# Kernel tuning notes

Measured on AMD Instinct MI355X. Metric: run time of the kernel, lower is better.

## Reference

```python
import jax, jax.numpy as jnp
import numpy as np

EPS = 1e-5  # matches module default eps


def setup_inputs() -> dict:
    key = jax.random.key(0)
    n, F = 4096, 256
    k1, k2, k3, k4, k5 = jax.random.split(key, 5)
    # Orthonormal eigenbasis (eigh of a symmetric Laplacian yields orthogonal V)
    V = jnp.linalg.qr(jax.random.normal(k1, (n, n), dtype=jnp.float32))[0]
    # Nonnegative Laplacian spectrum with lam[0] = 0 (module asserts sqrtlam[0] ~ 0)
    lam = jnp.sort(jax.random.uniform(k2, (n,), dtype=jnp.float32) * 4.0)
    lam = lam.at[0].set(0.0)
    x = jax.random.normal(k3, (n, F, 1), dtype=jnp.float32)
    y = jax.random.normal(k4, (n, F, 1), dtype=jnp.float32)
    t = jnp.float32(0.7)
    return {"x": x, "y": y, "t": t, "lam": lam, "V": V}


def reference(x, y, t, lam, V):
    # safe_sqrt: clamp tiny negatives (|lam|<eps) to zero before sqrt
    sqrtlam = jnp.sqrt(jnp.maximum(lam, 0.0))
    # P1 spectrum: cos(t * sqrt(lam))
    c = jnp.cos(t * sqrtlam)
    # P2 spectrum: sin(t*s)/s with limit t as s->0 (safe_P2_eigh)
    small = jnp.abs(sqrtlam) < EPS
    safe_s = jnp.where(small, 1.0, sqrtlam)
    p2 = jnp.where(small, t, jnp.sin(t * safe_s) / safe_s)

    def apply_spectral(d, sig):
        # (V diag(d) V^T) @ sig, contracted over node axis; sig: [n, F, C]
        vt_sig = jnp.einsum('ji,jfc->ifc', V, sig)          # V^T @ sig
        return jnp.einsum('ij,jfc->ifc', V, d[:, None, None] * vt_sig)

    # res1 + res2: P1 @ x + P2 @ y (the scatter-add message passing with all
    # nonzeros of the dense P matrices is exactly this dense mat-vec)
    return apply_spectral(c, x) + apply_spectral(p2, y)
```

## Files before the change

### kernel.cpp

```cpp
#include <hip/hip_runtime.h>

typedef __attribute__((ext_vector_type(8))) short short8;
typedef __attribute__((ext_vector_type(8))) unsigned short ushort8v;
typedef __attribute__((ext_vector_type(4))) float f32x4;

#define N_NODES 4096
#define N_FEAT  256

__device__ __forceinline__ unsigned short f2bf(float f) {
  union { float f; unsigned u; } a; a.f = f;
  unsigned r = a.u + 0x7FFFu + ((a.u >> 16) & 1u);
  return (unsigned short)(r >> 16);
}

__device__ __forceinline__ float bf2f(unsigned short u) {
  union { unsigned u; float f; } a; a.u = ((unsigned)u) << 16;
  return a.f;
}

__device__ __forceinline__ void gload_lds16(const void* g, void* l) {
  __builtin_amdgcn_global_load_lds(
      (const __attribute__((address_space(1))) void*)g,
      (__attribute__((address_space(3))) void*)l, 16, 0, 0);
}

__global__ __launch_bounds__(256) void prep_v_k(const float* __restrict__ V,
                                                unsigned short* __restrict__ Vbf,
                                                unsigned short* __restrict__ Vt) {
  __shared__ unsigned short tile[64][72];
  const int t = threadIdx.x;
  const int r = t >> 2, q = t & 3;
  const int gr = blockIdx.y * 64 + r;
  const int gc0 = blockIdx.x * 64;
#pragma unroll
  for (int i = 0; i < 4; ++i) {
    int c = q * 4 + i * 16;
    float4 v = *(const float4*)&V[(size_t)gr * N_NODES + gc0 + c];
    ushort4 u; u.x = f2bf(v.x); u.y = f2bf(v.y); u.z = f2bf(v.z); u.w = f2bf(v.w);
    *(ushort4*)&Vbf[(size_t)gr * N_NODES + gc0 + c] = u;
    tile[c + 0][r] = u.x; tile[c + 1][r] = u.y; tile[c + 2][r] = u.z; tile[c + 3][r] = u.w;
  }
  __syncthreads();
  const int r2 = t >> 2;
#pragma unroll
  for (int j = 0; j < 2; ++j) {
    int ms = q * 8 + j * 32;
    ushort8v u = *(const ushort8v*)&tile[r2][ms];
    *(ushort8v*)&Vt[(size_t)(gc0 + r2) * N_NODES + blockIdx.y * 64 + ms] = u;
  }
}

__global__ __launch_bounds__(256) void prep_xy_k(const float* __restrict__ x,
                                                 const float* __restrict__ y,
                                                 unsigned short* __restrict__ S2T) {
  __shared__ unsigned short tx[64][72];
  __shared__ unsigned short ty[64][72];
  const int t = threadIdx.x;
  const int r = t >> 2, q = t & 3;
  const int gj = blockIdx.y * 64 + r;
  const int gf0 = blockIdx.x * 64;
#pragma unroll
  for (int i = 0; i < 4; ++i) {
    int c = q * 4 + i * 16;
    float4 vx = *(const float4*)&x[(size_t)gj * N_FEAT + gf0 + c];
    float4 vy = *(const float4*)&y[(size_t)gj * N_FEAT + gf0 + c];
    tx[c + 0][r] = f2bf(vx.x); tx[c + 1][r] = f2bf(vx.y);
    tx[c + 2][r] = f2bf(vx.z); tx[c + 3][r] = f2bf(vx.w);
    ty[c + 0][r] = f2bf(vy.x); ty[c + 1][r] = f2bf(vy.y);
    ty[c + 2][r] = f2bf(vy.z); ty[c + 3][r] = f2bf(vy.w);
  }
  __syncthreads();
  const int f2 = t >> 2;
#pragma unroll
  for (int j = 0; j < 2; ++j) {
    int js = q * 8 + j * 32;
    ushort8v ux = *(const ushort8v*)&tx[f2][js];
    ushort8v uy = *(const ushort8v*)&ty[f2][js];
    *(ushort8v*)&S2T[(size_t)(2 * (gf0 + f2) + 0) * N_NODES + blockIdx.y * 64 + js] = ux;
    *(ushort8v*)&S2T[(size_t)(2 * (gf0 + f2) + 1) * N_NODES + blockIdx.y * 64 + js] = uy;
  }
}

template <int NTB>
__global__ __launch_bounds__(256, 3) void gemm_swz(const unsigned short* __restrict__ A,
                                                   const unsigned short* __restrict__ B,
                                                   unsigned short* __restrict__ part,
                                                   int K, int Kc, int Nn, size_t MN) {
  __shared__ unsigned short As[2][128 * 64];
  __shared__ unsigned short Bs[2][64 * 64];
  const int t = threadIdx.x;
  const int lane = t & 63, w = t >> 6;

  const unsigned L = blockIdx.x;
  const unsigned cx = L & 7u, j = L >> 3;
  const unsigned ntile = j & ((1u << NTB) - 1u);
  const unsigned group = cx * (128u >> NTB) + (j >> NTB);
  const unsigned mtile = group & 31u;
  const unsigned zz = group >> 5u;

  const int wr = (w >> 1) * 64;
  const int wc = (w & 1) * 32;
  const int l15 = lane & 15;
  const int lhi = lane >> 4;

  const size_t kbase = (size_t)zz * Kc;
  const size_t srcoff = (size_t)(lane >> 3) * K * 2 + (size_t)(((lane & 7) ^ (lane >> 3)) << 4);

  const char* Ag = (const char*)(A + (size_t)mtile * 128 * K + kbase);
  const char* Bg = (const char*)(B + (size_t)ntile * 64 * K + kbase);

  f32x4 acc[4][2];
#pragma unroll
  for (int mi = 0; mi < 4; ++mi)
#pragma unroll
    for (int ni = 0; ni < 2; ++ni) acc[mi][ni] = (f32x4){0.f, 0.f, 0.f, 0.f};

  auto STAGE = [&](int kt, int cur) {
    const size_t ko = (size_t)kt * 128;
#pragma unroll
    for (int q = 0; q < 4; ++q)
      gload_lds16(Ag + (size_t)(w * 4 + q) * 8 * K * 2 + srcoff + ko,
                  &As[cur][(w * 4 + q) * 512]);
#pragma unroll
    for (int q = 0; q < 2; ++q)
      gload_lds16(Bg + (size_t)(w * 2 + q) * 8 * K * 2 + srcoff + ko,
                  &Bs[cur][(w * 2 + q) * 512]);
  };

  auto COMPUTE = [&](int cur) {
    short8 a[4][2], b[2][2];
#pragma unroll
    for (int mi = 0; mi < 4; ++mi) {
      const int ar = wr + mi * 16 + l15;
#pragma unroll
      for (int ks = 0; ks < 2; ++ks)
        a[mi][ks] = *(const short8*)((const char*)&As[cur][0] + (size_t)ar * 128 +
                                     ((((ks << 2) | lhi) ^ (ar & 7)) << 4));
    }
#pragma unroll
    for (int ni = 0; ni < 2; ++ni) {
      const int br = wc + ni * 16 + l15;
#pragma unroll
      for (int ks = 0; ks < 2; ++ks)
        b[ni][ks] = *(const short8*)((const char*)&Bs[cur][0] + (size_t)br * 128 +
                                     ((((ks << 2) | lhi) ^ (br & 7)) << 4));
    }
#pragma unroll
    for (int ks = 0; ks < 2; ++ks)
#pragma unroll
      for (int mi = 0; mi < 4; ++mi)
#pragma unroll
        for (int ni = 0; ni < 2; ++ni)
          acc[mi][ni] = __builtin_amdgcn_mfma_f32_16x16x32_bf16(a[mi][ks], b[ni][ks],
                                                                acc[mi][ni], 0, 0, 0);
  };

  const int nkt = Kc >> 6;
  STAGE(0, 0);
  __syncthreads();
  int cur = 0;
  for (int kt = 0; kt < nkt - 1; ++kt) {
    STAGE(kt + 1, cur ^ 1);
    COMPUTE(cur);
    __syncthreads();
    cur ^= 1;
  }
  COMPUTE(cur);

  unsigned short* po = part + (size_t)zz * MN;
  const int m0 = mtile * 128 + wr + lhi * 4;
  const int n0 = ntile * 64 + wc + l15;
#pragma unroll
  for (int mi = 0; mi < 4; ++mi)
#pragma unroll
    for (int ni = 0; ni < 2; ++ni)
#pragma unroll
      for (int r = 0; r < 4; ++r)
        po[(size_t)(m0 + mi * 16 + r) * Nn + n0 + ni * 16] = f2bf(acc[mi][ni][r]);
}

__global__ __launch_bounds__(256) void reduce1_k(const unsigned short* __restrict__ part,
                                                 const float* __restrict__ lam,
                                                 const float* __restrict__ tp,
                                                 unsigned short* __restrict__ Zt) {
  __shared__ unsigned short zt[64][72];
  const int t = threadIdx.x;
  const int r = t >> 2, q = t & 3;
  const int m = blockIdx.y * 64 + r;
  const int n0 = blockIdx.x * 128;
  const float tv = tp[0];
  const float s = sqrtf(fmaxf(lam[m], 0.f));
  const float cv = cosf(tv * s);
  const float pv = (s < 1e-5f) ? tv : (sinf(tv * s) / s);
  float acc[16];
#pragma unroll
  for (int i = 0; i < 16; ++i) acc[i] = 0.f;
  for (int ks = 0; ks < 4; ++ks) {
    const unsigned short* p = part + ((size_t)ks * N_NODES + m) * 512 + n0;
#pragma unroll
    for (int i = 0; i < 8; ++i) {
      ushort4 u = *(const ushort4*)&p[q * 4 + i * 16];
      acc[2 * i + 0] += cv * bf2f(u.x) + pv * bf2f(u.y);
      acc[2 * i + 1] += cv * bf2f(u.z) + pv * bf2f(u.w);
    }
  }
#pragma unroll
  for (int i = 0; i < 8; ++i) {
    int f = q * 2 + i * 8;
    zt[f + 0][r] = f2bf(acc[2 * i + 0]);
    zt[f + 1][r] = f2bf(acc[2 * i + 1]);
  }
  __syncthreads();
  const int f2 = t >> 2;
  const int gf = blockIdx.x * 64 + f2;
#pragma unroll
  for (int w = 0; w < 2; ++w) {
    int js = q * 8 + w * 32;
    ushort8v u = *(const ushort8v*)&zt[f2][js];
    *(ushort8v*)&Zt[(size_t)gf * N_NODES + blockIdx.y * 64 + js] = u;
  }
}

__global__ __launch_bounds__(256) void reduce2_k(const unsigned short* __restrict__ part,
                                                 float* __restrict__ out) {
  const size_t e = ((size_t)blockIdx.x * 256 + threadIdx.x) * 4;
  float4 s = {0.f, 0.f, 0.f, 0.f};
#pragma unroll
  for (int ks = 0; ks < 8; ++ks) {
    ushort4 u = *(const ushort4*)&part[(size_t)ks * N_NODES * N_FEAT + e];
    s.x += bf2f(u.x); s.y += bf2f(u.y); s.z += bf2f(u.z); s.w += bf2f(u.w);
  }
  *(float4*)&out[e] = s;
}

extern "C" void kernel_launch(void* const* d_in, const int* in_sizes, int n_in,
                              void* d_out, int out_size, void* d_ws, size_t ws_size,
                              hipStream_t stream) {
  const float* x   = (const float*)d_in[0];
  const float* y   = (const float*)d_in[1];
  const float* tp  = (const float*)d_in[2];
  const float* lam = (const float*)d_in[3];
  const float* V   = (const float*)d_in[4];

  char* w = (char*)d_ws;
  unsigned short* Vbf  = (unsigned short*)w; w += (size_t)N_NODES * N_NODES * 2;
  unsigned short* Vtbf = (unsigned short*)w; w += (size_t)N_NODES * N_NODES * 2;
  unsigned short* S2T  = (unsigned short*)w; w += (size_t)512 * N_NODES * 2;
  unsigned short* Zt   = (unsigned short*)w; w += (size_t)N_FEAT * N_NODES * 2;
  unsigned short* partb = (unsigned short*)w; w += (size_t)4 * N_NODES * 512 * 2;

  prep_v_k<<<dim3(N_NODES / 64, N_NODES / 64), 256, 0, stream>>>(V, Vbf, Vtbf);
  prep_xy_k<<<dim3(N_FEAT / 64, N_NODES / 64), 256, 0, stream>>>(x, y, S2T);
  gemm_swz<3><<<1024, 256, 0, stream>>>(Vtbf, S2T, partb, N_NODES, 1024, 512,
                                        (size_t)N_NODES * 512);
  reduce1_k<<<dim3(512 / 128, N_NODES / 64), 256, 0, stream>>>(partb, lam, tp, Zt);
  gemm_swz<2><<<1024, 256, 0, stream>>>(Vbf, Zt, partb, N_NODES, 512, N_FEAT,
                                        (size_t)N_NODES * N_FEAT);
  reduce2_k<<<(N_NODES * N_FEAT) / 1024, 256, 0, stream>>>(partb, (float*)d_out);
}
```

Before: 192.6 us.

## Enlarge GEMM tiles to 128x128, drop double buffering, double split-K factor

The GEMM block tile grows from 128x64 to 128x128, so each wave now computes a 64x64 output with 16 accumulators and gets more reuse from each LDS load. The LDS double buffer is replaced by a single buffer with load, sync, compute, sync per k-step, which removes overlap between the global-to-LDS copy and the MFMA work. To keep 1024 blocks, the K split doubles (8 and 16 partials), so both reduce kernels read twice as many bf16 partial buffers and the partial workspace doubles.

```diff
diff --git a/kernel.cpp b/kernel.cpp
--- a/kernel.cpp
+++ b/kernel.cpp
@@ -86,20 +86,21 @@
                                                    const unsigned short* __restrict__ B,
                                                    unsigned short* __restrict__ part,
                                                    int K, int Kc, int Nn, size_t MN) {
-  __shared__ unsigned short As[2][128 * 64];
-  __shared__ unsigned short Bs[2][64 * 64];
+  __shared__ unsigned short As[128 * 64];
+  __shared__ unsigned short Bs[128 * 64];
   const int t = threadIdx.x;
   const int lane = t & 63, w = t >> 6;
 
   const unsigned L = blockIdx.x;
-  const unsigned cx = L & 7u, j = L >> 3;
+  const unsigned cx = L & 7u, j = L >> 3u;
   const unsigned ntile = j & ((1u << NTB) - 1u);
-  const unsigned group = cx * (128u >> NTB) + (j >> NTB);
+  const unsigned GPX = (gridDim.x >> 3) >> NTB;
+  const unsigned group = cx * GPX + (j >> NTB);
   const unsigned mtile = group & 31u;
   const unsigned zz = group >> 5u;
 
   const int wr = (w >> 1) * 64;
-  const int wc = (w & 1) * 32;
+  const int wc = (w & 1) * 64;
   const int l15 = lane & 15;
   const int lhi = lane >> 4;
 
@@ -107,73 +108,56 @@
   const size_t srcoff = (size_t)(lane >> 3) * K * 2 + (size_t)(((lane & 7) ^ (lane >> 3)) << 4);
 
   const char* Ag = (const char*)(A + (size_t)mtile * 128 * K + kbase);
-  const char* Bg = (const char*)(B + (size_t)ntile * 64 * K + kbase);
-
-  f32x4 acc[4][2];
+  const char* Bg = (const char*)(B + (size_t)ntile * 128 * K + kbase);
+
+  f32x4 acc[4][4];
 #pragma unroll
   for (int mi = 0; mi < 4; ++mi)
 #pragma unroll
-    for (int ni = 0; ni < 2; ++ni) acc[mi][ni] = (f32x4){0.f, 0.f, 0.f, 0.f};
-
-  auto STAGE = [&](int kt, int cur) {
+    for (int ni = 0; ni < 4; ++ni) acc[mi][ni] = (f32x4){0.f, 0.f, 0.f, 0.f};
+
+  const int nkt = Kc >> 6;
+  for (int kt = 0; kt < nkt; ++kt) {
     const size_t ko = (size_t)kt * 128;
 #pragma unroll
     for (int q = 0; q < 4; ++q)
-      gload_lds16(Ag + (size_t)(w * 4 + q) * 8 * K * 2 + srcoff + ko,
-                  &As[cur][(w * 4 + q) * 512]);
-#pragma unroll
-    for (int q = 0; q < 2; ++q)
-      gload_lds16(Bg + (size_t)(w * 2 + q) * 8 * K * 2 + srcoff + ko,
-                  &Bs[cur][(w * 2 + q) * 512]);
-  };
-
-  auto COMPUTE = [&](int cur) {
-    short8 a[4][2], b[2][2];
-#pragma unroll
-    for (int mi = 0; mi < 4; ++mi) {
-      const int ar = wr + mi * 16 + l15;
-#pragma unroll
-      for (int ks = 0; ks < 2; ++ks)
-        a[mi][ks] = *(const short8*)((const char*)&As[cur][0] + (size_t)ar * 128 +
-                                     ((((ks << 2) | lhi) ^ (ar & 7)) << 4));
+      gload_lds16(Ag + (size_t)(w * 4 + q) * 8 * K * 2 + srcoff + ko, &As[(w * 4 + q) * 512]);
+#pragma unroll
+    for (int q = 0; q < 4; ++q)
+      gload_lds16(Bg + (size_t)(w * 4 + q) * 8 * K * 2 + srcoff + ko, &Bs[(w * 4 + q) * 512]);
+    __syncthreads();
+#pragma unroll
+    for (int ks = 0; ks < 2; ++ks) {
+      short8 a[4], b[4];
+#pragma unroll
+      for (int mi = 0; mi < 4; ++mi) {
+        const int ar = wr + mi * 16 + l15;
+        a[mi] = *(const short8*)((const char*)As + (size_t)ar * 128 +
+                                 ((((ks << 2) | lhi) ^ (ar & 7)) << 4));
+      }
+#pragma unroll
+      for (int ni = 0; ni < 4; ++ni) {
+        const int br = wc + ni * 16 + l15;
+        b[ni] = *(const short8*)((const char*)Bs + (size_t)br * 128 +
+                                 ((((ks << 2) | lhi) ^ (br & 7)) << 4));
+      }
+#pragma unroll
+      for (int mi = 0; mi < 4; ++mi)
+#pragma unroll
+        for (int ni = 0; ni < 4; ++ni)
+          acc[mi][ni] = __builtin_amdgcn_mfma_f32_16x16x32_bf16(a[mi], b[ni],
+                                                                acc[mi][ni], 0, 0, 0);
     }
-#pragma unroll
-    for (int ni = 0; ni < 2; ++ni) {
-      const int br = wc + ni * 16 + l15;
-#pragma unroll
-      for (int ks = 0; ks < 2; ++ks)
-        b[ni][ks] = *(const short8*)((const char*)&Bs[cur][0] + (size_t)br * 128 +
-                                     ((((ks << 2) | lhi) ^ (br & 7)) << 4));
-    }
-#pragma unroll
-    for (int ks = 0; ks < 2; ++ks)
-#pragma unroll
-      for (int mi = 0; mi < 4; ++mi)
-#pragma unroll
-        for (int ni = 0; ni < 2; ++ni)
-          acc[mi][ni] = __builtin_amdgcn_mfma_f32_16x16x32_bf16(a[mi][ks], b[ni][ks],
-                                                                acc[mi][ni], 0, 0, 0);
-  };
-
-  const int nkt = Kc >> 6;
-  STAGE(0, 0);
-  __syncthreads();
-  int cur = 0;
-  for (int kt = 0; kt < nkt - 1; ++kt) {
-    STAGE(kt + 1, cur ^ 1);
-    COMPUTE(cur);
     __syncthreads();
-    cur ^= 1;
-  }
-  COMPUTE(cur);
+  }
 
   unsigned short* po = part + (size_t)zz * MN;
   const int m0 = mtile * 128 + wr + lhi * 4;
-  const int n0 = ntile * 64 + wc + l15;
+  const int n0 = ntile * 128 + wc + l15;
 #pragma unroll
   for (int mi = 0; mi < 4; ++mi)
 #pragma unroll
-    for (int ni = 0; ni < 2; ++ni)
+    for (int ni = 0; ni < 4; ++ni)
 #pragma unroll
       for (int r = 0; r < 4; ++r)
         po[(size_t)(m0 + mi * 16 + r) * Nn + n0 + ni * 16] = f2bf(acc[mi][ni][r]);
@@ -195,7 +179,7 @@
   float acc[16];
 #pragma unroll
   for (int i = 0; i < 16; ++i) acc[i] = 0.f;
-  for (int ks = 0; ks < 4; ++ks) {
+  for (int ks = 0; ks < 8; ++ks) {
     const unsigned short* p = part + ((size_t)ks * N_NODES + m) * 512 + n0;
 #pragma unroll
     for (int i = 0; i < 8; ++i) {
@@ -226,7 +210,7 @@
   const size_t e = ((size_t)blockIdx.x * 256 + threadIdx.x) * 4;
   float4 s = {0.f, 0.f, 0.f, 0.f};
 #pragma unroll
-  for (int ks = 0; ks < 8; ++ks) {
+  for (int ks = 0; ks < 16; ++ks) {
     ushort4 u = *(const ushort4*)&part[(size_t)ks * N_NODES * N_FEAT + e];
     s.x += bf2f(u.x); s.y += bf2f(u.y); s.z += bf2f(u.z); s.w += bf2f(u.w);
   }
@@ -247,14 +231,14 @@
   unsigned short* Vtbf = (unsigned short*)w; w += (size_t)N_NODES * N_NODES * 2;
   unsigned short* S2T  = (unsigned short*)w; w += (size_t)512 * N_NODES * 2;
   unsigned short* Zt   = (unsigned short*)w; w += (size_t)N_FEAT * N_NODES * 2;
-  unsigned short* partb = (unsigned short*)w; w += (size_t)4 * N_NODES * 512 * 2;
+  unsigned short* partb = (unsigned short*)w; w += (size_t)8 * N_NODES * 512 * 2;
 
   prep_v_k<<<dim3(N_NODES / 64, N_NODES / 64), 256, 0, stream>>>(V, Vbf, Vtbf);
   prep_xy_k<<<dim3(N_FEAT / 64, N_NODES / 64), 256, 0, stream>>>(x, y, S2T);
-  gemm_swz<3><<<1024, 256, 0, stream>>>(Vtbf, S2T, partb, N_NODES, 1024, 512,
+  gemm_swz<2><<<1024, 256, 0, stream>>>(Vtbf, S2T, partb, N_NODES, 512, 512,
                                         (size_t)N_NODES * 512);
   reduce1_k<<<dim3(512 / 128, N_NODES / 64), 256, 0, stream>>>(partb, lam, tp, Zt);
-  gemm_swz<2><<<1024, 256, 0, stream>>>(Vbf, Zt, partb, N_NODES, 512, N_FEAT,
+  gemm_swz<1><<<1024, 256, 0, stream>>>(Vbf, Zt, partb, N_NODES, 256, N_FEAT,
                                         (size_t)N_NODES * N_FEAT);
   reduce2_k<<<(N_NODES * N_FEAT) / 1024, 256, 0, stream>>>(partb, (float*)d_out);
 }
```

New measurement: 174.2 us. -9.5%, faster.
